# Kernel tuning notes

Measured on AMD Instinct MI355X. Metric: run time of the kernel, lower is better.

The kernel has to match this reference:

```python
import jax, jax.numpy as jnp
import numpy as np

NUM_HEADS = 16
HEAD_DIM = 64  # hidden_size 1024 / 16 heads


def setup_inputs() -> dict:
    key = jax.random.key(0)
    k1, k2, k3, k4 = jax.random.split(key, 4)
    B, S, Dm = 1, 2048, 1024
    scale = 1.0 / np.sqrt(Dm)
    return {
        "hidden_states": jax.random.normal(k1, (B, S, Dm), dtype=jnp.float32),
        "Wq": jax.random.normal(k2, (Dm, Dm), dtype=jnp.float32) * scale,
        "Wk": jax.random.normal(k3, (Dm, Dm), dtype=jnp.float32) * scale,
        "Wv": jax.random.normal(k4, (Dm, Dm), dtype=jnp.float32) * scale,
    }


def reference(hidden_states, Wq, Wk, Wv):
    # hidden_states: [B, S, Dm]; Wq/Wk/Wv: [Dm, Dm] (no bias)
    B, S, Dm = hidden_states.shape
    H, D = NUM_HEADS, HEAD_DIM
    q = (hidden_states @ Wq).reshape(B, S, H, D)
    k = (hidden_states @ Wk).reshape(B, S, H, D)
    v = (hidden_states @ Wv).reshape(B, S, H, D)
    # scaled dot-product scores: [B, H, Sq, Sk]
    scores = jnp.einsum("bqhd,bkhd->bhqk", q, k) / jnp.sqrt(jnp.float32(D))
    probs = jax.nn.softmax(scores, axis=-1)
    # context: [B, Sq, H, D] -> [B, Sq, H*D]
    context = jnp.einsum("bhqk,bkhd->bqhd", probs, v).reshape(B, S, H * D)
    # module permutes scores [B, Sq, Sk, H] -> [B, H, Sq, Sk]; we built that layout directly
    return context, probs
```

## Files before the change

kernel.cpp:

```cpp
#include <hip/hip_runtime.h>
#include <cstdint>
#include <cstddef>

#define SEQ 2048
#define DMODEL 1024
#define NHEADS 16
#define HDIM 64

typedef __attribute__((ext_vector_type(8))) short short8;
typedef __attribute__((ext_vector_type(4))) float floatx4;

__device__ __forceinline__ short f2bf(float f) {
  union { float f; uint32_t u; } x; x.f = f;
  uint32_t r = (x.u + 0x7FFFu + ((x.u >> 16) & 1u)) >> 16;
  return (short)(uint16_t)r;
}

__device__ __forceinline__ void gl_lds16(const short* g, short* l) {
  __builtin_amdgcn_global_load_lds((const __attribute__((address_space(1))) void*)g,
                                   (__attribute__((address_space(3))) void*)l, 16, 0, 0);
}

__global__ __launch_bounds__(256) void cast_bf16_kernel(const float* __restrict__ src,
                                                        short* __restrict__ dst, int n) {
  int i = blockIdx.x * 256 + threadIdx.x;
  if (i < n) dst[i] = f2bf(src[i]);
}

__global__ __launch_bounds__(256) void transpose_cast_kernel(const float* __restrict__ src,
                                                             short* __restrict__ dst) {
  __shared__ float tile[32][33];
  int tx = threadIdx.x, ty = threadIdx.y;
  int x = blockIdx.x * 32 + tx;
  int y0 = blockIdx.y * 32;
#pragma unroll
  for (int j = 0; j < 32; j += 8)
    tile[ty + j][tx] = src[(size_t)(y0 + ty + j) * DMODEL + x];
  __syncthreads();
  int xo = blockIdx.y * 32 + tx;
  int yo0 = blockIdx.x * 32;
#pragma unroll
  for (int j = 0; j < 32; j += 8)
    dst[(size_t)(yo0 + ty + j) * DMODEL + xo] = f2bf(tile[tx][ty + j]);
}

__global__ __launch_bounds__(256) void qkv_gemm_kernel(const short* __restrict__ Xb,
                                                       const short* __restrict__ Wt,
                                                       short* __restrict__ q,
                                                       short* __restrict__ k,
                                                       short* __restrict__ vT) {
  __shared__ short Abuf[128 * 32];
  __shared__ short Bbuf[128 * 32];
  int tid = threadIdx.x;
  int wave = tid >> 6, lane = tid & 63;
  int lr = lane & 15, quad = lane >> 4;
  int m0 = blockIdx.y * 128;
  int n0 = blockIdx.x * 128;
  int wr = wave >> 1, wc = wave & 1;

  const short* Ag = Xb + (size_t)(m0 + (tid >> 2)) * DMODEL + (tid & 3) * 8;
  const short* Bg = Wt + (size_t)(n0 + (tid >> 2)) * DMODEL + (tid & 3) * 8;
  short* Al = Abuf + wave * 512;
  short* Bl = Bbuf + wave * 512;

  floatx4 acc[4][4] = {};
  bool isV = (n0 >= 2 * DMODEL);

  for (int kb = 0; kb < DMODEL; kb += 32) {
    __syncthreads();
    gl_lds16(Ag + kb, Al);
    gl_lds16(Ag + kb + 64 * DMODEL, Al + 2048);
    gl_lds16(Bg + kb, Bl);
    gl_lds16(Bg + kb + 64 * DMODEL, Bl + 2048);
    __syncthreads();

    short8 a[4], b[4];
#pragma unroll
    for (int i = 0; i < 4; ++i) {
      a[i] = *(const short8*)(Abuf + (wr * 64 + i * 16 + lr) * 32 + quad * 8);
      b[i] = *(const short8*)(Bbuf + (wc * 64 + i * 16 + lr) * 32 + quad * 8);
    }
    if (isV) {
#pragma unroll
      for (int mi = 0; mi < 4; ++mi)
#pragma unroll
        for (int ni = 0; ni < 4; ++ni)
          acc[mi][ni] = __builtin_amdgcn_mfma_f32_16x16x32_bf16(b[ni], a[mi], acc[mi][ni], 0, 0, 0);
    } else {
#pragma unroll
      for (int mi = 0; mi < 4; ++mi)
#pragma unroll
        for (int ni = 0; ni < 4; ++ni)
          acc[mi][ni] = __builtin_amdgcn_mfma_f32_16x16x32_bf16(a[mi], b[ni], acc[mi][ni], 0, 0, 0);
    }
  }

  if (!isV) {
    short* out = (n0 < DMODEL) ? q : k;
    int nbase = n0 & (DMODEL - 1);
#pragma unroll
    for (int mi = 0; mi < 4; ++mi)
#pragma unroll
      for (int ni = 0; ni < 4; ++ni) {
        int n = nbase + wc * 64 + ni * 16 + lr;
        int hh = n >> 6, d = n & 63;
        size_t base = ((size_t)hh * SEQ + m0 + wr * 64 + mi * 16 + quad * 4) * HDIM + d;
#pragma unroll
        for (int r = 0; r < 4; ++r) out[base + (size_t)r * HDIM] = f2bf(acc[mi][ni][r]);
      }
  } else {
    int nbase = n0 - 2 * DMODEL;
#pragma unroll
    for (int mi = 0; mi < 4; ++mi) {
      int sidx = m0 + wr * 64 + mi * 16 + lr;
#pragma unroll
      for (int ni = 0; ni < 4; ++ni) {
        int n = nbase + wc * 64 + ni * 16 + quad * 4;
#pragma unroll
        for (int r = 0; r < 4; ++r) vT[(size_t)(n + r) * SEQ + sidx] = f2bf(acc[mi][ni][r]);
      }
    }
  }
}

#define PSTRF 132

__global__ __launch_bounds__(256) void attn_fused_kernel(const short* __restrict__ q,
                                                         const short* __restrict__ k,
                                                         const short* __restrict__ vT,
                                                         float* __restrict__ probs,
                                                         float* __restrict__ ctx) {
  __shared__ float pf[4][16 * PSTRF];
  __shared__ float partial[4][16][64];
  __shared__ float wred[4][16];

  int h = blockIdx.y;
  int m0 = blockIdx.x * 16;
  int wave = threadIdx.x >> 6, lane = threadIdx.x & 63;
  int lr = lane & 15, quad = lane >> 4;
  int nb = wave * 512;

  const short* Q = q + ((size_t)h * SEQ + m0 + lr) * HDIM + quad * 8;
  short8 qa0 = *(const short8*)(Q);
  short8 qa1 = *(const short8*)(Q + 32);

  const short* K = k + (size_t)h * SEQ * HDIM + quad * 8;

  floatx4 s[32];
#pragma unroll
  for (int f = 0; f < 32; ++f) {
    const short* Kr = K + (size_t)(nb + f * 16 + lr) * HDIM;
    short8 b0 = *(const short8*)(Kr);
    short8 b1 = *(const short8*)(Kr + 32);
    floatx4 t = {};
    t = __builtin_amdgcn_mfma_f32_16x16x32_bf16(qa0, b0, t, 0, 0, 0);
    s[f] = __builtin_amdgcn_mfma_f32_16x16x32_bf16(qa1, b1, t, 0, 0, 0);
  }

  float mrow[4] = {-3.4e38f, -3.4e38f, -3.4e38f, -3.4e38f};
#pragma unroll
  for (int f = 0; f < 32; ++f)
#pragma unroll
    for (int r = 0; r < 4; ++r) {
      s[f][r] *= 0.125f;
      mrow[r] = fmaxf(mrow[r], s[f][r]);
    }
#pragma unroll
  for (int off = 8; off >= 1; off >>= 1)
#pragma unroll
    for (int r = 0; r < 4; ++r) mrow[r] = fmaxf(mrow[r], __shfl_xor(mrow[r], off));
  if (lr == 0)
#pragma unroll
    for (int r = 0; r < 4; ++r) wred[wave][quad * 4 + r] = mrow[r];
  __syncthreads();
#pragma unroll
  for (int r = 0; r < 4; ++r) {
    int row = quad * 4 + r;
    mrow[r] = fmaxf(fmaxf(wred[0][row], wred[1][row]), fmaxf(wred[2][row], wred[3][row]));
  }
  __syncthreads();

  float srow[4] = {0.f, 0.f, 0.f, 0.f};
#pragma unroll
  for (int f = 0; f < 32; ++f)
#pragma unroll
    for (int r = 0; r < 4; ++r) {
      float e = __expf(s[f][r] - mrow[r]);
      s[f][r] = e;
      srow[r] += e;
    }
#pragma unroll
  for (int off = 8; off >= 1; off >>= 1)
#pragma unroll
    for (int r = 0; r < 4; ++r) srow[r] += __shfl_xor(srow[r], off);
  if (lr == 0)
#pragma unroll
    for (int r = 0; r < 4; ++r) wred[wave][quad * 4 + r] = srow[r];
  __syncthreads();
  float inv[4];
#pragma unroll
  for (int r = 0; r < 4; ++r) {
    int row = quad * 4 + r;
    inv[r] = 1.0f / (wred[0][row] + wred[1][row] + wred[2][row] + wred[3][row]);
  }

  float* pw = pf[wave];
  const short* Vb = vT + (size_t)h * HDIM * SEQ;
  floatx4 cacc[4] = {};
  int prow = lane >> 5;
  int pchunk = lane & 31;

#pragma unroll
  for (int c = 0; c < 4; ++c) {
#pragma unroll
    for (int fi = 0; fi < 8; ++fi) {
      int f = c * 8 + fi;
#pragma unroll
      for (int r = 0; r < 4; ++r)
        pw[(quad * 4 + r) * PSTRF + fi * 16 + lr] = s[f][r] * inv[r];
    }
#pragma unroll
    for (int i = 0; i < 8; ++i) {
      int row = i * 2 + prow;
      floatx4 v4 = *(const floatx4*)(pw + row * PSTRF + pchunk * 4);
      __builtin_nontemporal_store(
          v4, (floatx4*)(probs + ((size_t)h * SEQ + m0 + row) * SEQ + nb + c * 128 + pchunk * 4));
    }
#pragma unroll
    for (int kt = 0; kt < 128; kt += 32) {
      const float* pa = pw + lr * PSTRF + kt + quad * 8;
      floatx4 p0 = *(const floatx4*)(pa);
      floatx4 p1 = *(const floatx4*)(pa + 4);
      short8 a;
#pragma unroll
      for (int j = 0; j < 4; ++j) {
        a[j] = f2bf(p0[j]);
        a[4 + j] = f2bf(p1[j]);
      }
#pragma unroll
      for (int f = 0; f < 4; ++f) {
        short8 b = *(const short8*)(Vb + (size_t)(f * 16 + lr) * SEQ + nb + c * 128 + kt + quad * 8);
        cacc[f] = __builtin_amdgcn_mfma_f32_16x16x32_bf16(a, b, cacc[f], 0, 0, 0);
      }
    }
  }

#pragma unroll
  for (int f = 0; f < 4; ++f)
#pragma unroll
    for (int r = 0; r < 4; ++r) partial[wave][quad * 4 + r][f * 16 + lr] = cacc[f][r];
  __syncthreads();
  for (int e = threadIdx.x; e < 16 * 64; e += 256) {
    int m = e >> 6, d = e & 63;
    float v = partial[0][m][d] + partial[1][m][d] + partial[2][m][d] + partial[3][m][d];
    ctx[(size_t)(m0 + m) * DMODEL + h * HDIM + d] = v;
  }
}

extern "C" void kernel_launch(void* const* d_in, const int* in_sizes, int n_in,
                              void* d_out, int out_size, void* d_ws, size_t ws_size,
                              hipStream_t stream) {
  const float* X = (const float*)d_in[0];
  const float* Wq = (const float*)d_in[1];
  const float* Wk = (const float*)d_in[2];
  const float* Wv = (const float*)d_in[3];

  float* ctx = (float*)d_out;
  float* probs = (float*)d_out + (size_t)SEQ * DMODEL;

  short* Xb = (short*)d_ws;
  short* Wt = Xb + (size_t)SEQ * DMODEL;
  short* qb = Wt + (size_t)3 * DMODEL * DMODEL;
  short* kb = qb + (size_t)NHEADS * SEQ * HDIM;
  short* vT = kb + (size_t)NHEADS * SEQ * HDIM;

  cast_bf16_kernel<<<(SEQ * DMODEL + 255) / 256, 256, 0, stream>>>(X, Xb, SEQ * DMODEL);
  dim3 tb(32, 8), tg(32, 32);
  transpose_cast_kernel<<<tg, tb, 0, stream>>>(Wq, Wt);
  transpose_cast_kernel<<<tg, tb, 0, stream>>>(Wk, Wt + (size_t)DMODEL * DMODEL);
  transpose_cast_kernel<<<tg, tb, 0, stream>>>(Wv, Wt + (size_t)2 * DMODEL * DMODEL);

  qkv_gemm_kernel<<<dim3(3 * DMODEL / 128, SEQ / 128), 256, 0, stream>>>(Xb, Wt, qb, kb, vT);
  attn_fused_kernel<<<dim3(SEQ / 16, NHEADS), 256, 0, stream>>>(qb, kb, vT, probs, ctx);
}
```

Baseline: 447.7 us.

## Double-buffer QKV GEMM with smaller M tile; recompute scores with online softmax

```diff
diff --git a/kernel.cpp b/kernel.cpp
--- a/kernel.cpp
+++ b/kernel.cpp
@@ -49,75 +49,81 @@
                                                        short* __restrict__ q,
                                                        short* __restrict__ k,
                                                        short* __restrict__ vT) {
-  __shared__ short Abuf[128 * 32];
-  __shared__ short Bbuf[128 * 32];
+  __shared__ short Ab[2][64 * 32];
+  __shared__ short Bb[2][128 * 32];
   int tid = threadIdx.x;
   int wave = tid >> 6, lane = tid & 63;
   int lr = lane & 15, quad = lane >> 4;
-  int m0 = blockIdx.y * 128;
+  int m0 = blockIdx.y * 64;
   int n0 = blockIdx.x * 128;
   int wr = wave >> 1, wc = wave & 1;
 
   const short* Ag = Xb + (size_t)(m0 + (tid >> 2)) * DMODEL + (tid & 3) * 8;
   const short* Bg = Wt + (size_t)(n0 + (tid >> 2)) * DMODEL + (tid & 3) * 8;
-  short* Al = Abuf + wave * 512;
-  short* Bl = Bbuf + wave * 512;
-
-  floatx4 acc[4][4] = {};
   bool isV = (n0 >= 2 * DMODEL);
 
-  for (int kb = 0; kb < DMODEL; kb += 32) {
+  floatx4 acc[2][4] = {};
+
+  gl_lds16(Ag, Ab[0] + wave * 512);
+  gl_lds16(Bg, Bb[0] + wave * 512);
+  gl_lds16(Bg + 64 * DMODEL, Bb[0] + 2048 + wave * 512);
+  __syncthreads();
+
+  int cur = 0;
+  for (int t = 0; t < 32; ++t) {
+    if (t < 31) {
+      int kb = (t + 1) * 32;
+      gl_lds16(Ag + kb, Ab[cur ^ 1] + wave * 512);
+      gl_lds16(Bg + kb, Bb[cur ^ 1] + wave * 512);
+      gl_lds16(Bg + kb + 64 * DMODEL, Bb[cur ^ 1] + 2048 + wave * 512);
+    }
+    short8 a[2], b[4];
+#pragma unroll
+    for (int i = 0; i < 2; ++i)
+      a[i] = *(const short8*)(Ab[cur] + (wr * 32 + i * 16 + lr) * 32 + quad * 8);
+#pragma unroll
+    for (int j = 0; j < 4; ++j)
+      b[j] = *(const short8*)(Bb[cur] + (wc * 64 + j * 16 + lr) * 32 + quad * 8);
+    if (isV) {
+#pragma unroll
+      for (int i = 0; i < 2; ++i)
+#pragma unroll
+        for (int j = 0; j < 4; ++j)
+          acc[i][j] = __builtin_amdgcn_mfma_f32_16x16x32_bf16(b[j], a[i], acc[i][j], 0, 0, 0);
+    } else {
+#pragma unroll
+      for (int i = 0; i < 2; ++i)
+#pragma unroll
+        for (int j = 0; j < 4; ++j)
+          acc[i][j] = __builtin_amdgcn_mfma_f32_16x16x32_bf16(a[i], b[j], acc[i][j], 0, 0, 0);
+    }
     __syncthreads();
-    gl_lds16(Ag + kb, Al);
-    gl_lds16(Ag + kb + 64 * DMODEL, Al + 2048);
-    gl_lds16(Bg + kb, Bl);
-    gl_lds16(Bg + kb + 64 * DMODEL, Bl + 2048);
-    __syncthreads();
-
-    short8 a[4], b[4];
-#pragma unroll
-    for (int i = 0; i < 4; ++i) {
-      a[i] = *(const short8*)(Abuf + (wr * 64 + i * 16 + lr) * 32 + quad * 8);
-      b[i] = *(const short8*)(Bbuf + (wc * 64 + i * 16 + lr) * 32 + quad * 8);
-    }
-    if (isV) {
-#pragma unroll
-      for (int mi = 0; mi < 4; ++mi)
-#pragma unroll
-        for (int ni = 0; ni < 4; ++ni)
-          acc[mi][ni] = __builtin_amdgcn_mfma_f32_16x16x32_bf16(b[ni], a[mi], acc[mi][ni], 0, 0, 0);
-    } else {
-#pragma unroll
-      for (int mi = 0; mi < 4; ++mi)
-#pragma unroll
-        for (int ni = 0; ni < 4; ++ni)
-          acc[mi][ni] = __builtin_amdgcn_mfma_f32_16x16x32_bf16(a[mi], b[ni], acc[mi][ni], 0, 0, 0);
-    }
+    cur ^= 1;
   }
 
   if (!isV) {
     short* out = (n0 < DMODEL) ? q : k;
     int nbase = n0 & (DMODEL - 1);
 #pragma unroll
-    for (int mi = 0; mi < 4; ++mi)
-#pragma unroll
-      for (int ni = 0; ni < 4; ++ni) {
-        int n = nbase + wc * 64 + ni * 16 + lr;
+    for (int i = 0; i < 2; ++i)
+#pragma unroll
+      for (int j = 0; j < 4; ++j) {
+        int n = nbase + wc * 64 + j * 16 + lr;
         int hh = n >> 6, d = n & 63;
-        size_t base = ((size_t)hh * SEQ + m0 + wr * 64 + mi * 16 + quad * 4) * HDIM + d;
-#pragma unroll
-        for (int r = 0; r < 4; ++r) out[base + (size_t)r * HDIM] = f2bf(acc[mi][ni][r]);
+        size_t base = ((size_t)hh * SEQ + m0 + wr * 32 + i * 16 + quad * 4) * HDIM + d;
+#pragma unroll
+        for (int r = 0; r < 4; ++r) out[base + (size_t)r * HDIM] = f2bf(acc[i][j][r]);
       }
   } else {
     int nbase = n0 - 2 * DMODEL;
 #pragma unroll
-    for (int mi = 0; mi < 4; ++mi) {
-      int sidx = m0 + wr * 64 + mi * 16 + lr;
-#pragma unroll
-      for (int ni = 0; ni < 4; ++ni) {
-        int n = nbase + wc * 64 + ni * 16 + quad * 4;
-#pragma unroll
-        for (int r = 0; r < 4; ++r) vT[(size_t)(n + r) * SEQ + sidx] = f2bf(acc[mi][ni][r]);
+    for (int i = 0; i < 2; ++i) {
+      int sidx = m0 + wr * 32 + i * 16 + lr;
+#pragma unroll
+      for (int j = 0; j < 4; ++j) {
+        int n = nbase + wc * 64 + j * 16 + quad * 4;
+#pragma unroll
+        for (int r = 0; r < 4; ++r) vT[(size_t)(n + r) * SEQ + sidx] = f2bf(acc[i][j][r]);
       }
     }
   }
@@ -125,14 +131,13 @@
 
 #define PSTRF 132
 
-__global__ __launch_bounds__(256) void attn_fused_kernel(const short* __restrict__ q,
-                                                         const short* __restrict__ k,
-                                                         const short* __restrict__ vT,
-                                                         float* __restrict__ probs,
-                                                         float* __restrict__ ctx) {
+__global__ __launch_bounds__(256, 4) void attn_fused_kernel(const short* __restrict__ q,
+                                                            const short* __restrict__ k,
+                                                            const short* __restrict__ vT,
+                                                            float* __restrict__ probs,
+                                                            float* __restrict__ ctx) {
   __shared__ float pf[4][16 * PSTRF];
-  __shared__ float partial[4][16][64];
-  __shared__ float wred[4][16];
+  __shared__ float wm[4][16], wl[4][16];
 
   int h = blockIdx.y;
   int m0 = blockIdx.x * 16;
@@ -143,65 +148,65 @@
   const short* Q = q + ((size_t)h * SEQ + m0 + lr) * HDIM + quad * 8;
   short8 qa0 = *(const short8*)(Q);
   short8 qa1 = *(const short8*)(Q + 32);
-
   const short* K = k + (size_t)h * SEQ * HDIM + quad * 8;
 
-  floatx4 s[32];
-#pragma unroll
-  for (int f = 0; f < 32; ++f) {
-    const short* Kr = K + (size_t)(nb + f * 16 + lr) * HDIM;
-    short8 b0 = *(const short8*)(Kr);
-    short8 b1 = *(const short8*)(Kr + 32);
-    floatx4 t = {};
-    t = __builtin_amdgcn_mfma_f32_16x16x32_bf16(qa0, b0, t, 0, 0, 0);
-    s[f] = __builtin_amdgcn_mfma_f32_16x16x32_bf16(qa1, b1, t, 0, 0, 0);
-  }
-
-  float mrow[4] = {-3.4e38f, -3.4e38f, -3.4e38f, -3.4e38f};
-#pragma unroll
-  for (int f = 0; f < 32; ++f)
+  float mrow[4], lrow[4];
+#pragma unroll
+  for (int r = 0; r < 4; ++r) { mrow[r] = -3.4e38f; lrow[r] = 0.f; }
+
+#pragma unroll 1
+  for (int c = 0; c < 4; ++c) {
+    floatx4 s[8];
+#pragma unroll
+    for (int f = 0; f < 8; ++f) {
+      const short* Kr = K + (size_t)(nb + c * 128 + f * 16 + lr) * HDIM;
+      short8 b0 = *(const short8*)(Kr);
+      short8 b1 = *(const short8*)(Kr + 32);
+      floatx4 t = {};
+      t = __builtin_amdgcn_mfma_f32_16x16x32_bf16(qa0, b0, t, 0, 0, 0);
+      s[f] = __builtin_amdgcn_mfma_f32_16x16x32_bf16(qa1, b1, t, 0, 0, 0);
+    }
 #pragma unroll
     for (int r = 0; r < 4; ++r) {
-      s[f][r] *= 0.125f;
-      mrow[r] = fmaxf(mrow[r], s[f][r]);
-    }
+      float cm = s[0][r];
+#pragma unroll
+      for (int f = 1; f < 8; ++f) cm = fmaxf(cm, s[f][r]);
+      cm *= 0.125f;
+      float mn = fmaxf(mrow[r], cm);
+      float sum = 0.f;
+#pragma unroll
+      for (int f = 0; f < 8; ++f) sum += __expf(s[f][r] * 0.125f - mn);
+      lrow[r] = lrow[r] * __expf(mrow[r] - mn) + sum;
+      mrow[r] = mn;
+    }
+  }
+
 #pragma unroll
   for (int off = 8; off >= 1; off >>= 1)
 #pragma unroll
-    for (int r = 0; r < 4; ++r) mrow[r] = fmaxf(mrow[r], __shfl_xor(mrow[r], off));
+    for (int r = 0; r < 4; ++r) {
+      float om = __shfl_xor(mrow[r], off);
+      float ol = __shfl_xor(lrow[r], off);
+      float mn = fmaxf(mrow[r], om);
+      lrow[r] = lrow[r] * __expf(mrow[r] - mn) + ol * __expf(om - mn);
+      mrow[r] = mn;
+    }
   if (lr == 0)
 #pragma unroll
-    for (int r = 0; r < 4; ++r) wred[wave][quad * 4 + r] = mrow[r];
-  __syncthreads();
+    for (int r = 0; r < 4; ++r) {
+      wm[wave][quad * 4 + r] = mrow[r];
+      wl[wave][quad * 4 + r] = lrow[r];
+    }
+  __syncthreads();
+  float inv[4];
 #pragma unroll
   for (int r = 0; r < 4; ++r) {
     int row = quad * 4 + r;
-    mrow[r] = fmaxf(fmaxf(wred[0][row], wred[1][row]), fmaxf(wred[2][row], wred[3][row]));
-  }
-  __syncthreads();
-
-  float srow[4] = {0.f, 0.f, 0.f, 0.f};
-#pragma unroll
-  for (int f = 0; f < 32; ++f)
-#pragma unroll
-    for (int r = 0; r < 4; ++r) {
-      float e = __expf(s[f][r] - mrow[r]);
-      s[f][r] = e;
-      srow[r] += e;
-    }
-#pragma unroll
-  for (int off = 8; off >= 1; off >>= 1)
-#pragma unroll
-    for (int r = 0; r < 4; ++r) srow[r] += __shfl_xor(srow[r], off);
-  if (lr == 0)
-#pragma unroll
-    for (int r = 0; r < 4; ++r) wred[wave][quad * 4 + r] = srow[r];
-  __syncthreads();
-  float inv[4];
-#pragma unroll
-  for (int r = 0; r < 4; ++r) {
-    int row = quad * 4 + r;
-    inv[r] = 1.0f / (wred[0][row] + wred[1][row] + wred[2][row] + wred[3][row]);
+    float m4 = fmaxf(fmaxf(wm[0][row], wm[1][row]), fmaxf(wm[2][row], wm[3][row]));
+    float l4 = wl[0][row] * __expf(wm[0][row] - m4) + wl[1][row] * __expf(wm[1][row] - m4) +
+               wl[2][row] * __expf(wm[2][row] - m4) + wl[3][row] * __expf(wm[3][row] - m4);
+    mrow[r] = m4;
+    inv[r] = 1.0f / l4;
   }
 
   float* pw = pf[wave];
@@ -210,15 +215,23 @@
   int prow = lane >> 5;
   int pchunk = lane & 31;
 
-#pragma unroll
+#pragma unroll 1
   for (int c = 0; c < 4; ++c) {
-#pragma unroll
-    for (int fi = 0; fi < 8; ++fi) {
-      int f = c * 8 + fi;
+    floatx4 s[8];
+#pragma unroll
+    for (int f = 0; f < 8; ++f) {
+      const short* Kr = K + (size_t)(nb + c * 128 + f * 16 + lr) * HDIM;
+      short8 b0 = *(const short8*)(Kr);
+      short8 b1 = *(const short8*)(Kr + 32);
+      floatx4 t = {};
+      t = __builtin_amdgcn_mfma_f32_16x16x32_bf16(qa0, b0, t, 0, 0, 0);
+      s[f] = __builtin_amdgcn_mfma_f32_16x16x32_bf16(qa1, b1, t, 0, 0, 0);
+    }
+#pragma unroll
+    for (int f = 0; f < 8; ++f)
 #pragma unroll
       for (int r = 0; r < 4; ++r)
-        pw[(quad * 4 + r) * PSTRF + fi * 16 + lr] = s[f][r] * inv[r];
-    }
+        pw[(quad * 4 + r) * PSTRF + f * 16 + lr] = __expf(s[f][r] * 0.125f - mrow[r]) * inv[r];
 #pragma unroll
     for (int i = 0; i < 8; ++i) {
       int row = i * 2 + prow;
@@ -245,14 +258,15 @@
     }
   }
 
+  float* part = pf[wave];
 #pragma unroll
   for (int f = 0; f < 4; ++f)
 #pragma unroll
-    for (int r = 0; r < 4; ++r) partial[wave][quad * 4 + r][f * 16 + lr] = cacc[f][r];
+    for (int r = 0; r < 4; ++r) part[(quad * 4 + r) * 64 + f * 16 + lr] = cacc[f][r];
   __syncthreads();
   for (int e = threadIdx.x; e < 16 * 64; e += 256) {
     int m = e >> 6, d = e & 63;
-    float v = partial[0][m][d] + partial[1][m][d] + partial[2][m][d] + partial[3][m][d];
+    float v = pf[0][m * 64 + d] + pf[1][m * 64 + d] + pf[2][m * 64 + d] + pf[3][m * 64 + d];
     ctx[(size_t)(m0 + m) * DMODEL + h * HDIM + d] = v;
   }
 }
@@ -280,6 +294,6 @@
   transpose_cast_kernel<<<tg, tb, 0, stream>>>(Wk, Wt + (size_t)DMODEL * DMODEL);
   transpose_cast_kernel<<<tg, tb, 0, stream>>>(Wv, Wt + (size_t)2 * DMODEL * DMODEL);
 
-  qkv_gemm_kernel<<<dim3(3 * DMODEL / 128, SEQ / 128), 256, 0, stream>>>(Xb, Wt, qb, kb, vT);
+  qkv_gemm_kernel<<<dim3(3 * DMODEL / 128, SEQ / 64), 256, 0, stream>>>(Xb, Wt, qb, kb, vT);
   attn_fused_kernel<<<dim3(SEQ / 16, NHEADS), 256, 0, stream>>>(qb, kb, vT, probs, ctx);
 }
```

Measured after the change: 453.0 us. Within noise of the previous version (+1.2%).
